# Optimization experiments

Hardware: AMD Instinct MI355X
Metric: run time of the kernel (lower is better)

The kernel has to match this reference:

```python
import jax, jax.numpy as jnp
import numpy as np

# SamplesLoss(loss='sinkhorn', p=1, blur=0.05): entropic regularization eps = blur**p = 0.05,
# debiased Sinkhorn divergence S(a,b) = OT(a,b) - 0.5*OT(a,a) - 0.5*OT(b,b).
EPS = 0.05
N_ITER = 50
N_POINTS = 32


def _cost(X, Y):
    # p=1 cost: Euclidean distance. X:[B,N,D] Y:[B,M,D] -> [B,N,M]
    d2 = jnp.sum((X[:, :, None, :] - Y[:, None, :, :]) ** 2, axis=-1)
    return jnp.sqrt(d2 + 1e-12)


def _ot(X, Y):
    # log-domain Sinkhorn with uniform weights; returns dual cost <mu,f>+<nu,g> per batch.
    B, N, _ = X.shape
    M = Y.shape[1]
    C = _cost(X, Y)  # [B,N,M]
    log_mu = jnp.full((B, N), -np.log(N), C.dtype)
    log_nu = jnp.full((B, M), -np.log(M), C.dtype)

    def body(carry, _):
        f, g = carry
        f = -EPS * jax.nn.logsumexp((g[:, None, :] - C) / EPS + log_nu[:, None, :], axis=2)
        g = -EPS * jax.nn.logsumexp((f[:, :, None] - C) / EPS + log_mu[:, :, None], axis=1)
        return (f, g), None

    init = (jnp.zeros((B, N), C.dtype), jnp.zeros((B, M), C.dtype))
    (f, g), _ = jax.lax.scan(body, init, None, length=N_ITER)
    return jnp.mean(f, axis=-1) + jnp.mean(g, axis=-1)  # uniform weights => mean


def _sinkhorn_div(X, Y):
    return _ot(X, Y) - 0.5 * _ot(X, X) - 0.5 * _ot(Y, Y)


def _encode(x, W, edge_index):
    # simple 1-layer GCN-style encoder: linear + mean neighbor aggregation + self, ReLU
    h = x @ W  # [n_nodes, emb_dim]
    src, dst = edge_index[0], edge_index[1]
    n = x.shape[0]
    agg = jax.ops.segment_sum(h[src], dst, num_segments=n)
    deg = jax.ops.segment_sum(jnp.ones(src.shape, h.dtype), dst, num_segments=n)
    return jax.nn.relu(h + agg / jnp.maximum(deg, 1.0)[:, None])


def setup_inputs() -> dict:
    key = jax.random.key(0)
    k1, k2, k3, k4, k5 = jax.random.split(key, 5)
    n_nodes, d_feat, emb_dim = 50000, 128, 256
    n_edges, n_pairs = 800000, 8192
    x = jax.random.normal(k1, (n_nodes, d_feat), jnp.float32)
    W = jax.random.normal(k2, (d_feat, emb_dim), jnp.float32) / np.sqrt(d_feat)
    edge_index = jax.random.randint(k3, (2, n_edges), 0, n_nodes, jnp.int64)
    pairs = jax.random.randint(k4, (2, n_pairs), 0, n_nodes, jnp.int64)
    graph_dist = jax.random.uniform(k5, (n_pairs,), jnp.float32, 1.0, 5.0)
    return {"x": x, "W": W, "edge_index": edge_index, "pairs": pairs,
            "graph_dist": graph_dist}


def reference(x, W, edge_index, pairs, graph_dist):
    z = _encode(x, W, edge_index)                       # [n_nodes, emb_dim]
    B = pairs.shape[1]
    Xa = z[pairs[0]].reshape(B, N_POINTS, -1)           # [B, n_points, space_dim]
    Xb = z[pairs[1]].reshape(B, N_POINTS, -1)
    distance = _sinkhorn_div(Xa, Xb)                    # = -score_pairs
    distortion = jnp.abs(distance - graph_dist) / graph_dist
    return jnp.mean(distortion)
```

## Files before the change

kernel.cpp:

```cpp
#include <hip/hip_runtime.h>

#define N_NODES 50000
#define N_EDGES 800000
#define N_PAIRS 8192
#define N_SLOTS (2 * N_PAIRS)
#define CAP     64

#define INV_EPS   20.0f
#define LOG2E_F   1.4426950408889634f
#define LN2_F     0.6931471805599453f
#define LN32_F    3.4657359027997265f
#define EPS_F     0.05f

typedef float f2 __attribute__((ext_vector_type(2)));

__global__ void k_mark(const int* __restrict__ pairs, int* __restrict__ flags) {
    int t = blockIdx.x * 256 + threadIdx.x;
    if (t < N_SLOTS) flags[pairs[t]] = 1;
}

__global__ __launch_bounds__(256) void k_scatter(
        const int* __restrict__ eidx, const int* __restrict__ flags,
        int* __restrict__ cnt, int* __restrict__ bucket) {
    int t = blockIdx.x * 256 + threadIdx.x;
    int dst = eidx[N_EDGES + t];
    if (!flags[dst]) return;
    int pos = atomicAdd(&cnt[dst], 1);
    if (pos < CAP) bucket[dst * CAP + pos] = eidx[t];
}

__global__ __launch_bounds__(256) void k_gemm(
        const int* __restrict__ pairs, const float* __restrict__ x,
        const int* __restrict__ cnt, const int* __restrict__ bucket,
        const float* __restrict__ W, float* __restrict__ Z) {
    __shared__ __align__(16) float Us[16 * 128];
    int sbase = blockIdx.x * 16;
    int t = threadIdx.x;
    int wave = t >> 6, lane = t & 63;

    #pragma unroll
    for (int rr = 0; rr < 4; ++rr) {
        int r = wave * 4 + rr;
        int node = pairs[sbase + r];
        int n = cnt[node];
        int m = (n < CAP) ? n : CAP;
        const int* bk = bucket + node * CAP;
        float ax = 0.0f, ay = 0.0f;
        int k = 0;
        for (; k + 4 <= m; k += 4) {
            int s0 = bk[k], s1 = bk[k + 1], s2 = bk[k + 2], s3 = bk[k + 3];
            float2 v0 = *(const float2*)(x + (size_t)s0 * 128 + lane * 2);
            float2 v1 = *(const float2*)(x + (size_t)s1 * 128 + lane * 2);
            float2 v2 = *(const float2*)(x + (size_t)s2 * 128 + lane * 2);
            float2 v3 = *(const float2*)(x + (size_t)s3 * 128 + lane * 2);
            ax += (v0.x + v1.x) + (v2.x + v3.x);
            ay += (v0.y + v1.y) + (v2.y + v3.y);
        }
        for (; k < m; ++k) {
            int s0 = bk[k];
            float2 v0 = *(const float2*)(x + (size_t)s0 * 128 + lane * 2);
            ax += v0.x;
            ay += v0.y;
        }
        float rdeg = 1.0f / fmaxf((float)n, 1.0f);
        float2 xv = *(const float2*)(x + (size_t)node * 128 + lane * 2);
        float2 o;
        o.x = fmaf(ax, rdeg, xv.x);
        o.y = fmaf(ay, rdeg, xv.y);
        *(float2*)(Us + r * 128 + lane * 2) = o;
    }
    __syncthreads();

    int jq = t & 63;
    int rq = t >> 6;
    float acc[4][4] = {};
    const float4* Wv = (const float4*)W;

    for (int k4 = 0; k4 < 32; ++k4) {
        float4 wv[4];
        #pragma unroll
        for (int i = 0; i < 4; ++i) wv[i] = Wv[(size_t)(k4 * 4 + i) * 64 + jq];
        #pragma unroll
        for (int r = 0; r < 4; ++r) {
            float4 uv = *(const float4*)(Us + (rq * 4 + r) * 128 + k4 * 4);
            float uk0 = uv.x, uk1 = uv.y, uk2 = uv.z, uk3 = uv.w;
            acc[r][0] = fmaf(uk0, wv[0].x, acc[r][0]);
            acc[r][1] = fmaf(uk0, wv[0].y, acc[r][1]);
            acc[r][2] = fmaf(uk0, wv[0].z, acc[r][2]);
            acc[r][3] = fmaf(uk0, wv[0].w, acc[r][3]);
            acc[r][0] = fmaf(uk1, wv[1].x, acc[r][0]);
            acc[r][1] = fmaf(uk1, wv[1].y, acc[r][1]);
            acc[r][2] = fmaf(uk1, wv[1].z, acc[r][2]);
            acc[r][3] = fmaf(uk1, wv[1].w, acc[r][3]);
            acc[r][0] = fmaf(uk2, wv[2].x, acc[r][0]);
            acc[r][1] = fmaf(uk2, wv[2].y, acc[r][1]);
            acc[r][2] = fmaf(uk2, wv[2].z, acc[r][2]);
            acc[r][3] = fmaf(uk2, wv[2].w, acc[r][3]);
            acc[r][0] = fmaf(uk3, wv[3].x, acc[r][0]);
            acc[r][1] = fmaf(uk3, wv[3].y, acc[r][1]);
            acc[r][2] = fmaf(uk3, wv[3].z, acc[r][2]);
            acc[r][3] = fmaf(uk3, wv[3].w, acc[r][3]);
        }
    }

    #pragma unroll
    for (int r = 0; r < 4; ++r) {
        float4 o;
        o.x = fmaxf(acc[r][0], 0.0f);
        o.y = fmaxf(acc[r][1], 0.0f);
        o.z = fmaxf(acc[r][2], 0.0f);
        o.w = fmaxf(acc[r][3], 0.0f);
        *(float4*)(Z + (size_t)(sbase + rq * 4 + r) * 256 + jq * 4) = o;
    }
}

__global__ __launch_bounds__(256) void k_sinkhorn(
        const float* __restrict__ Z, float* __restrict__ dist) {
    __shared__ __align__(16) float sX[4][256];
    __shared__ __align__(16) float sY[4][256];
    __shared__ __align__(16) float sf[4][32];
    __shared__ __align__(16) float sg[4][32];
    __shared__ __align__(16) float su[4][32];
    __shared__ __align__(16) float sv[4][32];

    int w = threadIdx.x >> 6;
    int lane = threadIdx.x & 63;
    int task = blockIdx.x * 4 + w;
    int b = task / 3;
    int kind = task - 3 * b;
    int sx = (kind == 2) ? (N_PAIRS + b) : b;
    int sy = (kind == 1) ? b : (N_PAIRS + b);

    *(float4*)(&sX[w][lane * 4]) = ((const float4*)(Z + (size_t)sx * 256))[lane];
    *(float4*)(&sY[w][lane * 4]) = ((const float4*)(Z + (size_t)sy * 256))[lane];
    sg[w][lane & 31] = 0.0f;

    const float CSCALE = -INV_EPS * LOG2E_F;
    const float CBIAS  = -LN32_F * LOG2E_F;

    int i_r = lane & 31, jh = lane >> 5;
    int j_c = lane & 31, ih = lane >> 5;

    f2 CrowV[8], CcolV[8];
    {
        const f2* xp = (const f2*)(&sX[w][i_r * 8]);
        f2 x0 = xp[0], x1 = xp[1], x2 = xp[2], x3 = xp[3];
        #pragma unroll
        for (int t = 0; t < 16; ++t) {
            int j = jh * 16 + t;
            const f2* yp = (const f2*)(&sY[w][j * 8]);
            f2 d, s2;
            d = x0 - yp[0]; s2 = d * d;
            d = x1 - yp[1]; s2 = __builtin_elementwise_fma(d, d, s2);
            d = x2 - yp[2]; s2 = __builtin_elementwise_fma(d, d, s2);
            d = x3 - yp[3]; s2 = __builtin_elementwise_fma(d, d, s2);
            float d2 = s2.x + s2.y + 1e-12f;
            CrowV[t >> 1][t & 1] = fmaf(__builtin_amdgcn_sqrtf(d2), CSCALE, CBIAS);
        }
        const f2* yp = (const f2*)(&sY[w][j_c * 8]);
        f2 y0 = yp[0], y1 = yp[1], y2 = yp[2], y3 = yp[3];
        #pragma unroll
        for (int t = 0; t < 16; ++t) {
            int i = ih * 16 + t;
            const f2* qp = (const f2*)(&sX[w][i * 8]);
            f2 d, s2;
            d = qp[0] - y0; s2 = d * d;
            d = qp[1] - y1; s2 = __builtin_elementwise_fma(d, d, s2);
            d = qp[2] - y2; s2 = __builtin_elementwise_fma(d, d, s2);
            d = qp[3] - y3; s2 = __builtin_elementwise_fma(d, d, s2);
            float d2 = s2.x + s2.y + 1e-12f;
            CcolV[t >> 1][t & 1] = fmaf(__builtin_amdgcn_sqrtf(d2), CSCALE, CBIAS);
        }
    }

    float ft = 0.0f, gt = 0.0f;

    #pragma unroll 1
    for (int it = 0; it < 2; ++it) {
        {
            const float4* gp = (const float4*)(&sg[w][jh * 16]);
            float4 G0 = gp[0], G1 = gp[1], G2 = gp[2], G3 = gp[3];
            f2 gv[8] = {f2{G0.x, G0.y}, f2{G0.z, G0.w}, f2{G1.x, G1.y}, f2{G1.z, G1.w},
                        f2{G2.x, G2.y}, f2{G2.z, G2.w}, f2{G3.x, G3.y}, f2{G3.z, G3.w}};
            f2 val[8], m2 = f2{-1e30f, -1e30f};
            #pragma unroll
            for (int t2 = 0; t2 < 8; ++t2) {
                val[t2] = gv[t2] + CrowV[t2];
                m2 = __builtin_elementwise_max(m2, val[t2]);
            }
            float m = fmaxf(m2.x, m2.y);
            m = fmaxf(m, __shfl_xor(m, 32));
            f2 mm = f2{m, m};
            float s0 = 0.0f, s1 = 0.0f;
            #pragma unroll
            for (int t2 = 0; t2 < 8; ++t2) {
                f2 e = val[t2] - mm;
                s0 += __builtin_amdgcn_exp2f(e.x);
                s1 += __builtin_amdgcn_exp2f(e.y);
            }
            float s = s0 + s1;
            s += __shfl_xor(s, 32);
            ft = -(m + __builtin_amdgcn_logf(s));
        }
        sf[w][lane & 31] = ft;
        {
            const float4* fp = (const float4*)(&sf[w][ih * 16]);
            float4 F0 = fp[0], F1 = fp[1], F2 = fp[2], F3 = fp[3];
            f2 fv[8] = {f2{F0.x, F0.y}, f2{F0.z, F0.w}, f2{F1.x, F1.y}, f2{F1.z, F1.w},
                        f2{F2.x, F2.y}, f2{F2.z, F2.w}, f2{F3.x, F3.y}, f2{F3.z, F3.w}};
            f2 val[8], m2 = f2{-1e30f, -1e30f};
            #pragma unroll
            for (int t2 = 0; t2 < 8; ++t2) {
                val[t2] = fv[t2] + CcolV[t2];
                m2 = __builtin_elementwise_max(m2, val[t2]);
            }
            float m = fmaxf(m2.x, m2.y);
            m = fmaxf(m, __shfl_xor(m, 32));
            f2 mm = f2{m, m};
            float s0 = 0.0f, s1 = 0.0f;
            #pragma unroll
            for (int t2 = 0; t2 < 8; ++t2) {
                f2 e = val[t2] - mm;
                s0 += __builtin_amdgcn_exp2f(e.x);
                s1 += __builtin_amdgcn_exp2f(e.y);
            }
            float s = s0 + s1;
            s += __shfl_xor(s, 32);
            gt = -(m + __builtin_amdgcn_logf(s));
        }
        sg[w][lane & 31] = gt;
    }

    f2 KR2[8], KC2[8];
    float ureg = 1.0f, vreg = 1.0f;

    auto absorb = [&]() {
        const float4* gp = (const float4*)(&sg[w][jh * 16]);
        float4 G0 = gp[0], G1 = gp[1], G2 = gp[2], G3 = gp[3];
        f2 gv[8] = {f2{G0.x, G0.y}, f2{G0.z, G0.w}, f2{G1.x, G1.y}, f2{G1.z, G1.w},
                    f2{G2.x, G2.y}, f2{G2.z, G2.w}, f2{G3.x, G3.y}, f2{G3.z, G3.w}};
        f2 ftv = f2{ft, ft};
        #pragma unroll
        for (int t2 = 0; t2 < 8; ++t2) {
            f2 a = (gv[t2] + CrowV[t2]) + ftv;
            KR2[t2].x = __builtin_amdgcn_exp2f(a.x);
            KR2[t2].y = __builtin_amdgcn_exp2f(a.y);
        }
        const float4* fp = (const float4*)(&sf[w][ih * 16]);
        float4 F0 = fp[0], F1 = fp[1], F2 = fp[2], F3 = fp[3];
        f2 fv[8] = {f2{F0.x, F0.y}, f2{F0.z, F0.w}, f2{F1.x, F1.y}, f2{F1.z, F1.w},
                    f2{F2.x, F2.y}, f2{F2.z, F2.w}, f2{F3.x, F3.y}, f2{F3.z, F3.w}};
        f2 gtv = f2{gt, gt};
        #pragma unroll
        for (int t2 = 0; t2 < 8; ++t2) {
            f2 a = (fv[t2] + CcolV[t2]) + gtv;
            KC2[t2].x = __builtin_amdgcn_exp2f(a.x);
            KC2[t2].y = __builtin_amdgcn_exp2f(a.y);
        }
        sv[w][lane & 31] = 1.0f;
        ureg = 1.0f;
        vreg = 1.0f;
    };

    const int blens[5] = {6, 6, 12, 12, 12};
    absorb();
    #pragma unroll 1
    for (int blk = 0; blk < 5; ++blk) {
        int L = blens[blk];
        #pragma unroll 2
        for (int s6 = 0; s6 < L; ++s6) {
            {
                const float4* vp = (const float4*)(&sv[w][jh * 16]);
                float4 A0 = vp[0], A1 = vp[1], A2 = vp[2], A3 = vp[3];
                f2 acc0 = KR2[0] * f2{A0.x, A0.y};
                f2 acc1 = KR2[1] * f2{A0.z, A0.w};
                acc0 = __builtin_elementwise_fma(KR2[2], f2{A1.x, A1.y}, acc0);
                acc1 = __builtin_elementwise_fma(KR2[3], f2{A1.z, A1.w}, acc1);
                acc0 = __builtin_elementwise_fma(KR2[4], f2{A2.x, A2.y}, acc0);
                acc1 = __builtin_elementwise_fma(KR2[5], f2{A2.z, A2.w}, acc1);
                acc0 = __builtin_elementwise_fma(KR2[6], f2{A3.x, A3.y}, acc0);
                acc1 = __builtin_elementwise_fma(KR2[7], f2{A3.z, A3.w}, acc1);
                f2 a = acc0 + acc1;
                float S = a.x + a.y;
                S += __shfl_xor(S, 32);
                ureg = __builtin_amdgcn_rcpf(S);
            }
            su[w][lane & 31] = ureg;
            {
                const float4* up = (const float4*)(&su[w][ih * 16]);
                float4 A0 = up[0], A1 = up[1], A2 = up[2], A3 = up[3];
                f2 acc0 = KC2[0] * f2{A0.x, A0.y};
                f2 acc1 = KC2[1] * f2{A0.z, A0.w};
                acc0 = __builtin_elementwise_fma(KC2[2], f2{A1.x, A1.y}, acc0);
                acc1 = __builtin_elementwise_fma(KC2[3], f2{A1.z, A1.w}, acc1);
                acc0 = __builtin_elementwise_fma(KC2[4], f2{A2.x, A2.y}, acc0);
                acc1 = __builtin_elementwise_fma(KC2[5], f2{A2.z, A2.w}, acc1);
                acc0 = __builtin_elementwise_fma(KC2[6], f2{A3.x, A3.y}, acc0);
                acc1 = __builtin_elementwise_fma(KC2[7], f2{A3.z, A3.w}, acc1);
                f2 a = acc0 + acc1;
                float T = a.x + a.y;
                T += __shfl_xor(T, 32);
                vreg = __builtin_amdgcn_rcpf(T);
            }
            sv[w][lane & 31] = vreg;
        }
        if (blk < 4) {
            ft += __builtin_amdgcn_logf(ureg);
            gt += __builtin_amdgcn_logf(vreg);
            sf[w][lane & 31] = ft;
            sg[w][lane & 31] = gt;
            absorb();
        }
    }
    ft += __builtin_amdgcn_logf(ureg);
    gt += __builtin_amdgcn_logf(vreg);

    float v = ft + gt;
    #pragma unroll
    for (int off = 32; off > 0; off >>= 1) v += __shfl_xor(v, off);
    if (lane == 0) {
        float cost = v * (EPS_F * LN2_F / 64.0f);
        float wgt = (kind == 0) ? 1.0f : -0.5f;
        unsafeAtomicAdd(&dist[b], wgt * cost);
    }
}

__global__ void k_finalize(const float* __restrict__ dist,
                           const float* __restrict__ gd, float* __restrict__ out) {
    __shared__ float red[256];
    float s = 0.0f;
    for (int i = threadIdx.x; i < N_PAIRS; i += 256) {
        float g = gd[i];
        s += fabsf(dist[i] - g) / g;
    }
    red[threadIdx.x] = s;
    __syncthreads();
    for (int o = 128; o > 0; o >>= 1) {
        if (threadIdx.x < o) red[threadIdx.x] += red[threadIdx.x + o];
        __syncthreads();
    }
    if (threadIdx.x == 0) out[0] = red[0] * (1.0f / N_PAIRS);
}

extern "C" void kernel_launch(void* const* d_in, const int* in_sizes, int n_in,
                              void* d_out, int out_size, void* d_ws, size_t ws_size,
                              hipStream_t stream) {
    const float* x    = (const float*)d_in[0];
    const float* W    = (const float*)d_in[1];
    const int*   eidx = (const int*)d_in[2];
    const int*   pair = (const int*)d_in[3];
    const float* gd   = (const float*)d_in[4];

    char* ws = (char*)d_ws;
    size_t off = 0;
    int*   cnt    = (int*)  (ws + off); off += (size_t)N_NODES * 4;
    int*   flags  = (int*)  (ws + off); off += (size_t)N_NODES * 4;
    float* dist   = (float*)(ws + off); off += (size_t)N_PAIRS * 4;
    size_t zero_bytes = off;
    int*   bucket = (int*)  (ws + off); off += (size_t)N_NODES * CAP * 4;
    float* Z      = (float*)(ws + off); off += (size_t)N_SLOTS * 256 * 4;

    hipMemsetAsync(d_ws, 0, zero_bytes, stream);
    k_mark    <<<(N_SLOTS + 255) / 256, 256, 0, stream>>>(pair, flags);
    k_scatter <<<N_EDGES / 256, 256, 0, stream>>>(eidx, flags, cnt, bucket);
    k_gemm    <<<N_SLOTS / 16, 256, 0, stream>>>(pair, x, cnt, bucket, W, Z);
    k_sinkhorn<<<(3 * N_PAIRS) / 4, 256, 0, stream>>>(Z, dist);
    k_finalize<<<1, 256, 0, stream>>>(dist, gd, (float*)d_out);
}
```

Baseline: 292.7 us.

## Specialize symmetric self-OT Sinkhorn tasks to half-wave symmetric iterations

The Sinkhorn kernel now splits blocks into cross-pair tasks (X vs Y) and self tasks (X vs X, Y vs Y). Self tasks use the symmetry of the cost matrix, so a single scaling vector updated by one matvec per half-step covers the problem, and each 64-lane wave handles both self-OT problems of a pair, one per 32-lane half. The total number of waves drops from three per pair to two, with less work per self problem. The risk is numerical: the symmetric single-vector iteration and its final averaging of the last two iterates must match the alternating f/g updates of the reference.

```diff
diff --git a/kernel.cpp b/kernel.cpp
--- a/kernel.cpp
+++ b/kernel.cpp
@@ -116,212 +116,314 @@
 
 __global__ __launch_bounds__(256) void k_sinkhorn(
         const float* __restrict__ Z, float* __restrict__ dist) {
-    __shared__ __align__(16) float sX[4][256];
-    __shared__ __align__(16) float sY[4][256];
-    __shared__ __align__(16) float sf[4][32];
-    __shared__ __align__(16) float sg[4][32];
-    __shared__ __align__(16) float su[4][32];
-    __shared__ __align__(16) float sv[4][32];
+    __shared__ __align__(16) float smem[4][640];
 
     int w = threadIdx.x >> 6;
     int lane = threadIdx.x & 63;
-    int task = blockIdx.x * 4 + w;
-    int b = task / 3;
-    int kind = task - 3 * b;
-    int sx = (kind == 2) ? (N_PAIRS + b) : b;
-    int sy = (kind == 1) ? b : (N_PAIRS + b);
-
-    *(float4*)(&sX[w][lane * 4]) = ((const float4*)(Z + (size_t)sx * 256))[lane];
-    *(float4*)(&sY[w][lane * 4]) = ((const float4*)(Z + (size_t)sy * 256))[lane];
-    sg[w][lane & 31] = 0.0f;
-
     const float CSCALE = -INV_EPS * LOG2E_F;
     const float CBIAS  = -LN32_F * LOG2E_F;
 
-    int i_r = lane & 31, jh = lane >> 5;
-    int j_c = lane & 31, ih = lane >> 5;
-
-    f2 CrowV[8], CcolV[8];
-    {
-        const f2* xp = (const f2*)(&sX[w][i_r * 8]);
-        f2 x0 = xp[0], x1 = xp[1], x2 = xp[2], x3 = xp[3];
-        #pragma unroll
-        for (int t = 0; t < 16; ++t) {
-            int j = jh * 16 + t;
-            const f2* yp = (const f2*)(&sY[w][j * 8]);
-            f2 d, s2;
-            d = x0 - yp[0]; s2 = d * d;
-            d = x1 - yp[1]; s2 = __builtin_elementwise_fma(d, d, s2);
-            d = x2 - yp[2]; s2 = __builtin_elementwise_fma(d, d, s2);
-            d = x3 - yp[3]; s2 = __builtin_elementwise_fma(d, d, s2);
-            float d2 = s2.x + s2.y + 1e-12f;
-            CrowV[t >> 1][t & 1] = fmaf(__builtin_amdgcn_sqrtf(d2), CSCALE, CBIAS);
-        }
-        const f2* yp = (const f2*)(&sY[w][j_c * 8]);
-        f2 y0 = yp[0], y1 = yp[1], y2 = yp[2], y3 = yp[3];
-        #pragma unroll
-        for (int t = 0; t < 16; ++t) {
-            int i = ih * 16 + t;
-            const f2* qp = (const f2*)(&sX[w][i * 8]);
-            f2 d, s2;
-            d = qp[0] - y0; s2 = d * d;
-            d = qp[1] - y1; s2 = __builtin_elementwise_fma(d, d, s2);
-            d = qp[2] - y2; s2 = __builtin_elementwise_fma(d, d, s2);
-            d = qp[3] - y3; s2 = __builtin_elementwise_fma(d, d, s2);
-            float d2 = s2.x + s2.y + 1e-12f;
-            CcolV[t >> 1][t & 1] = fmaf(__builtin_amdgcn_sqrtf(d2), CSCALE, CBIAS);
-        }
-    }
-
-    float ft = 0.0f, gt = 0.0f;
-
-    #pragma unroll 1
-    for (int it = 0; it < 2; ++it) {
+    if (blockIdx.x < 2048) {
+        float* sX = &smem[w][0];
+        float* sY = &smem[w][256];
+        float* sf = &smem[w][512];
+        float* sg = &smem[w][544];
+        float* su = &smem[w][576];
+        float* sv = &smem[w][608];
+
+        int b = blockIdx.x * 4 + w;
+        int sx = b, sy = N_PAIRS + b;
+
+        *(float4*)(&sX[lane * 4]) = ((const float4*)(Z + (size_t)sx * 256))[lane];
+        *(float4*)(&sY[lane * 4]) = ((const float4*)(Z + (size_t)sy * 256))[lane];
+        sg[lane & 31] = 0.0f;
+
+        int i_r = lane & 31, jh = lane >> 5;
+        int j_c = lane & 31, ih = lane >> 5;
+
+        f2 CrowV[8], CcolV[8];
         {
-            const float4* gp = (const float4*)(&sg[w][jh * 16]);
+            const f2* xp = (const f2*)(&sX[i_r * 8]);
+            f2 x0 = xp[0], x1 = xp[1], x2 = xp[2], x3 = xp[3];
+            #pragma unroll
+            for (int t = 0; t < 16; ++t) {
+                int j = jh * 16 + t;
+                const f2* yp = (const f2*)(&sY[j * 8]);
+                f2 d, s2;
+                d = x0 - yp[0]; s2 = d * d;
+                d = x1 - yp[1]; s2 = __builtin_elementwise_fma(d, d, s2);
+                d = x2 - yp[2]; s2 = __builtin_elementwise_fma(d, d, s2);
+                d = x3 - yp[3]; s2 = __builtin_elementwise_fma(d, d, s2);
+                float d2 = s2.x + s2.y + 1e-12f;
+                CrowV[t >> 1][t & 1] = fmaf(__builtin_amdgcn_sqrtf(d2), CSCALE, CBIAS);
+            }
+            const f2* yp = (const f2*)(&sY[j_c * 8]);
+            f2 y0 = yp[0], y1 = yp[1], y2 = yp[2], y3 = yp[3];
+            #pragma unroll
+            for (int t = 0; t < 16; ++t) {
+                int i = ih * 16 + t;
+                const f2* qp = (const f2*)(&sX[i * 8]);
+                f2 d, s2;
+                d = qp[0] - y0; s2 = d * d;
+                d = qp[1] - y1; s2 = __builtin_elementwise_fma(d, d, s2);
+                d = qp[2] - y2; s2 = __builtin_elementwise_fma(d, d, s2);
+                d = qp[3] - y3; s2 = __builtin_elementwise_fma(d, d, s2);
+                float d2 = s2.x + s2.y + 1e-12f;
+                CcolV[t >> 1][t & 1] = fmaf(__builtin_amdgcn_sqrtf(d2), CSCALE, CBIAS);
+            }
+        }
+
+        float ft = 0.0f, gt = 0.0f;
+
+        #pragma unroll 1
+        for (int it = 0; it < 2; ++it) {
+            {
+                const float4* gp = (const float4*)(&sg[jh * 16]);
+                float4 G0 = gp[0], G1 = gp[1], G2 = gp[2], G3 = gp[3];
+                f2 gv[8] = {f2{G0.x, G0.y}, f2{G0.z, G0.w}, f2{G1.x, G1.y}, f2{G1.z, G1.w},
+                            f2{G2.x, G2.y}, f2{G2.z, G2.w}, f2{G3.x, G3.y}, f2{G3.z, G3.w}};
+                f2 val[8], m2 = f2{-1e30f, -1e30f};
+                #pragma unroll
+                for (int t2 = 0; t2 < 8; ++t2) {
+                    val[t2] = gv[t2] + CrowV[t2];
+                    m2 = __builtin_elementwise_max(m2, val[t2]);
+                }
+                float m = fmaxf(m2.x, m2.y);
+                m = fmaxf(m, __shfl_xor(m, 32));
+                f2 mm = f2{m, m};
+                float s0 = 0.0f, s1 = 0.0f;
+                #pragma unroll
+                for (int t2 = 0; t2 < 8; ++t2) {
+                    f2 e = val[t2] - mm;
+                    s0 += __builtin_amdgcn_exp2f(e.x);
+                    s1 += __builtin_amdgcn_exp2f(e.y);
+                }
+                float s = s0 + s1;
+                s += __shfl_xor(s, 32);
+                ft = -(m + __builtin_amdgcn_logf(s));
+            }
+            sf[lane & 31] = ft;
+            {
+                const float4* fp = (const float4*)(&sf[ih * 16]);
+                float4 F0 = fp[0], F1 = fp[1], F2 = fp[2], F3 = fp[3];
+                f2 fv[8] = {f2{F0.x, F0.y}, f2{F0.z, F0.w}, f2{F1.x, F1.y}, f2{F1.z, F1.w},
+                            f2{F2.x, F2.y}, f2{F2.z, F2.w}, f2{F3.x, F3.y}, f2{F3.z, F3.w}};
+                f2 val[8], m2 = f2{-1e30f, -1e30f};
+                #pragma unroll
+                for (int t2 = 0; t2 < 8; ++t2) {
+                    val[t2] = fv[t2] + CcolV[t2];
+                    m2 = __builtin_elementwise_max(m2, val[t2]);
+                }
+                float m = fmaxf(m2.x, m2.y);
+                m = fmaxf(m, __shfl_xor(m, 32));
+                f2 mm = f2{m, m};
+                float s0 = 0.0f, s1 = 0.0f;
+                #pragma unroll
+                for (int t2 = 0; t2 < 8; ++t2) {
+                    f2 e = val[t2] - mm;
+                    s0 += __builtin_amdgcn_exp2f(e.x);
+                    s1 += __builtin_amdgcn_exp2f(e.y);
+                }
+                float s = s0 + s1;
+                s += __shfl_xor(s, 32);
+                gt = -(m + __builtin_amdgcn_logf(s));
+            }
+            sg[lane & 31] = gt;
+        }
+
+        f2 KR2[8], KC2[8];
+        float ureg = 1.0f, vreg = 1.0f;
+
+        auto absorb = [&]() {
+            const float4* gp = (const float4*)(&sg[jh * 16]);
             float4 G0 = gp[0], G1 = gp[1], G2 = gp[2], G3 = gp[3];
             f2 gv[8] = {f2{G0.x, G0.y}, f2{G0.z, G0.w}, f2{G1.x, G1.y}, f2{G1.z, G1.w},
                         f2{G2.x, G2.y}, f2{G2.z, G2.w}, f2{G3.x, G3.y}, f2{G3.z, G3.w}};
-            f2 val[8], m2 = f2{-1e30f, -1e30f};
+            f2 ftv = f2{ft, ft};
             #pragma unroll
             for (int t2 = 0; t2 < 8; ++t2) {
-                val[t2] = gv[t2] + CrowV[t2];
-                m2 = __builtin_elementwise_max(m2, val[t2]);
-            }
-            float m = fmaxf(m2.x, m2.y);
-            m = fmaxf(m, __shfl_xor(m, 32));
-            f2 mm = f2{m, m};
-            float s0 = 0.0f, s1 = 0.0f;
-            #pragma unroll
-            for (int t2 = 0; t2 < 8; ++t2) {
-                f2 e = val[t2] - mm;
-                s0 += __builtin_amdgcn_exp2f(e.x);
-                s1 += __builtin_amdgcn_exp2f(e.y);
-            }
-            float s = s0 + s1;
-            s += __shfl_xor(s, 32);
-            ft = -(m + __builtin_amdgcn_logf(s));
-        }
-        sf[w][lane & 31] = ft;
-        {
-            const float4* fp = (const float4*)(&sf[w][ih * 16]);
+                f2 a = (gv[t2] + CrowV[t2]) + ftv;
+                KR2[t2].x = __builtin_amdgcn_exp2f(a.x);
+                KR2[t2].y = __builtin_amdgcn_exp2f(a.y);
+            }
+            const float4* fp = (const float4*)(&sf[ih * 16]);
             float4 F0 = fp[0], F1 = fp[1], F2 = fp[2], F3 = fp[3];
             f2 fv[8] = {f2{F0.x, F0.y}, f2{F0.z, F0.w}, f2{F1.x, F1.y}, f2{F1.z, F1.w},
                         f2{F2.x, F2.y}, f2{F2.z, F2.w}, f2{F3.x, F3.y}, f2{F3.z, F3.w}};
-            f2 val[8], m2 = f2{-1e30f, -1e30f};
+            f2 gtv = f2{gt, gt};
             #pragma unroll
             for (int t2 = 0; t2 < 8; ++t2) {
-                val[t2] = fv[t2] + CcolV[t2];
-                m2 = __builtin_elementwise_max(m2, val[t2]);
-            }
-            float m = fmaxf(m2.x, m2.y);
-            m = fmaxf(m, __shfl_xor(m, 32));
-            f2 mm = f2{m, m};
-            float s0 = 0.0f, s1 = 0.0f;
+                f2 a = (fv[t2] + CcolV[t2]) + gtv;
+                KC2[t2].x = __builtin_amdgcn_exp2f(a.x);
+                KC2[t2].y = __builtin_amdgcn_exp2f(a.y);
+            }
+            sv[lane & 31] = 1.0f;
+            ureg = 1.0f;
+            vreg = 1.0f;
+        };
+
+        const int blens[5] = {6, 6, 12, 12, 12};
+        absorb();
+        #pragma unroll 1
+        for (int blk = 0; blk < 5; ++blk) {
+            int L = blens[blk];
+            #pragma unroll 2
+            for (int s6 = 0; s6 < L; ++s6) {
+                {
+                    const float4* vp = (const float4*)(&sv[jh * 16]);
+                    float4 A0 = vp[0], A1 = vp[1], A2 = vp[2], A3 = vp[3];
+                    f2 acc0 = KR2[0] * f2{A0.x, A0.y};
+                    f2 acc1 = KR2[1] * f2{A0.z, A0.w};
+                    acc0 = __builtin_elementwise_fma(KR2[2], f2{A1.x, A1.y}, acc0);
+                    acc1 = __builtin_elementwise_fma(KR2[3], f2{A1.z, A1.w}, acc1);
+                    acc0 = __builtin_elementwise_fma(KR2[4], f2{A2.x, A2.y}, acc0);
+                    acc1 = __builtin_elementwise_fma(KR2[5], f2{A2.z, A2.w}, acc1);
+                    acc0 = __builtin_elementwise_fma(KR2[6], f2{A3.x, A3.y}, acc0);
+                    acc1 = __builtin_elementwise_fma(KR2[7], f2{A3.z, A3.w}, acc1);
+                    f2 a = acc0 + acc1;
+                    float S = a.x + a.y;
+                    S += __shfl_xor(S, 32);
+                    ureg = __builtin_amdgcn_rcpf(S);
+                }
+                su[lane & 31] = ureg;
+                {
+                    const float4* up = (const float4*)(&su[ih * 16]);
+                    float4 A0 = up[0], A1 = up[1], A2 = up[2], A3 = up[3];
+                    f2 acc0 = KC2[0] * f2{A0.x, A0.y};
+                    f2 acc1 = KC2[1] * f2{A0.z, A0.w};
+                    acc0 = __builtin_elementwise_fma(KC2[2], f2{A1.x, A1.y}, acc0);
+                    acc1 = __builtin_elementwise_fma(KC2[3], f2{A1.z, A1.w}, acc1);
+                    acc0 = __builtin_elementwise_fma(KC2[4], f2{A2.x, A2.y}, acc0);
+                    acc1 = __builtin_elementwise_fma(KC2[5], f2{A2.z, A2.w}, acc1);
+                    acc0 = __builtin_elementwise_fma(KC2[6], f2{A3.x, A3.y}, acc0);
+                    acc1 = __builtin_elementwise_fma(KC2[7], f2{A3.z, A3.w}, acc1);
+                    f2 a = acc0 + acc1;
+                    float T = a.x + a.y;
+                    T += __shfl_xor(T, 32);
+                    vreg = __builtin_amdgcn_rcpf(T);
+                }
+                sv[lane & 31] = vreg;
+            }
+            if (blk < 4) {
+                ft += __builtin_amdgcn_logf(ureg);
+                gt += __builtin_amdgcn_logf(vreg);
+                sf[lane & 31] = ft;
+                sg[lane & 31] = gt;
+                absorb();
+            }
+        }
+        ft += __builtin_amdgcn_logf(ureg);
+        gt += __builtin_amdgcn_logf(vreg);
+
+        float v = ft + gt;
+        #pragma unroll
+        for (int off = 32; off > 0; off >>= 1) v += __shfl_xor(v, off);
+        if (lane == 0) {
+            float cost = v * (EPS_F * LN2_F / 64.0f);
+            unsafeAtomicAdd(&dist[b], cost);
+        }
+    } else {
+        int h = lane >> 5, i = lane & 31;
+        int P = (blockIdx.x - 2048) * 4 + w;
+        int src = h ? (N_PAIRS + P) : P;
+
+        float* sP  = &smem[w][h * 256];
+        float* swv = &smem[w][512];
+        float* spv = &smem[w][576];
+
+        {
+            const float4* zp = (const float4*)(Z + (size_t)src * 256);
+            *(float4*)(&sP[i * 8])     = zp[i * 2];
+            *(float4*)(&sP[i * 8 + 4]) = zp[i * 2 + 1];
+        }
+
+        f2 CV[16];
+        {
+            const f2* xp = (const f2*)(&sP[i * 8]);
+            f2 x0 = xp[0], x1 = xp[1], x2 = xp[2], x3 = xp[3];
             #pragma unroll
-            for (int t2 = 0; t2 < 8; ++t2) {
-                f2 e = val[t2] - mm;
-                s0 += __builtin_amdgcn_exp2f(e.x);
-                s1 += __builtin_amdgcn_exp2f(e.y);
-            }
-            float s = s0 + s1;
-            s += __shfl_xor(s, 32);
-            gt = -(m + __builtin_amdgcn_logf(s));
-        }
-        sg[w][lane & 31] = gt;
-    }
-
-    f2 KR2[8], KC2[8];
-    float ureg = 1.0f, vreg = 1.0f;
-
-    auto absorb = [&]() {
-        const float4* gp = (const float4*)(&sg[w][jh * 16]);
-        float4 G0 = gp[0], G1 = gp[1], G2 = gp[2], G3 = gp[3];
-        f2 gv[8] = {f2{G0.x, G0.y}, f2{G0.z, G0.w}, f2{G1.x, G1.y}, f2{G1.z, G1.w},
-                    f2{G2.x, G2.y}, f2{G2.z, G2.w}, f2{G3.x, G3.y}, f2{G3.z, G3.w}};
-        f2 ftv = f2{ft, ft};
+            for (int j = 0; j < 32; ++j) {
+                const f2* yp = (const f2*)(&sP[j * 8]);
+                f2 d, s2;
+                d = x0 - yp[0]; s2 = d * d;
+                d = x1 - yp[1]; s2 = __builtin_elementwise_fma(d, d, s2);
+                d = x2 - yp[2]; s2 = __builtin_elementwise_fma(d, d, s2);
+                d = x3 - yp[3]; s2 = __builtin_elementwise_fma(d, d, s2);
+                float d2 = s2.x + s2.y + 1e-12f;
+                CV[j >> 1][j & 1] = fmaf(__builtin_amdgcn_sqrtf(d2), CSCALE, CBIAS);
+            }
+        }
+
+        float pp = 0.0f, E = 1.0f, wcur = 1.0f, wprev = 1.0f;
+        f2 KV[16];
         #pragma unroll
-        for (int t2 = 0; t2 < 8; ++t2) {
-            f2 a = (gv[t2] + CrowV[t2]) + ftv;
-            KR2[t2].x = __builtin_amdgcn_exp2f(a.x);
-            KR2[t2].y = __builtin_amdgcn_exp2f(a.y);
-        }
-        const float4* fp = (const float4*)(&sf[w][ih * 16]);
-        float4 F0 = fp[0], F1 = fp[1], F2 = fp[2], F3 = fp[3];
-        f2 fv[8] = {f2{F0.x, F0.y}, f2{F0.z, F0.w}, f2{F1.x, F1.y}, f2{F1.z, F1.w},
-                    f2{F2.x, F2.y}, f2{F2.z, F2.w}, f2{F3.x, F3.y}, f2{F3.z, F3.w}};
-        f2 gtv = f2{gt, gt};
-        #pragma unroll
-        for (int t2 = 0; t2 < 8; ++t2) {
-            f2 a = (fv[t2] + CcolV[t2]) + gtv;
-            KC2[t2].x = __builtin_amdgcn_exp2f(a.x);
-            KC2[t2].y = __builtin_amdgcn_exp2f(a.y);
-        }
-        sv[w][lane & 31] = 1.0f;
-        ureg = 1.0f;
-        vreg = 1.0f;
-    };
-
-    const int blens[5] = {6, 6, 12, 12, 12};
-    absorb();
-    #pragma unroll 1
-    for (int blk = 0; blk < 5; ++blk) {
-        int L = blens[blk];
-        #pragma unroll 2
-        for (int s6 = 0; s6 < L; ++s6) {
-            {
-                const float4* vp = (const float4*)(&sv[w][jh * 16]);
-                float4 A0 = vp[0], A1 = vp[1], A2 = vp[2], A3 = vp[3];
-                f2 acc0 = KR2[0] * f2{A0.x, A0.y};
-                f2 acc1 = KR2[1] * f2{A0.z, A0.w};
-                acc0 = __builtin_elementwise_fma(KR2[2], f2{A1.x, A1.y}, acc0);
-                acc1 = __builtin_elementwise_fma(KR2[3], f2{A1.z, A1.w}, acc1);
-                acc0 = __builtin_elementwise_fma(KR2[4], f2{A2.x, A2.y}, acc0);
-                acc1 = __builtin_elementwise_fma(KR2[5], f2{A2.z, A2.w}, acc1);
-                acc0 = __builtin_elementwise_fma(KR2[6], f2{A3.x, A3.y}, acc0);
-                acc1 = __builtin_elementwise_fma(KR2[7], f2{A3.z, A3.w}, acc1);
+        for (int t = 0; t < 16; ++t) {
+            KV[t].x = __builtin_amdgcn_exp2f(CV[t].x);
+            KV[t].y = __builtin_amdgcn_exp2f(CV[t].y);
+        }
+        swv[lane] = 1.0f;
+
+        const int blens[9] = {4, 12, 12, 12, 12, 12, 12, 12, 12};
+        #pragma unroll 1
+        for (int blk = 0; blk < 9; ++blk) {
+            int L = blens[blk];
+            #pragma unroll 2
+            for (int s = 0; s < L; ++s) {
+                const float4* wp = (const float4*)(&swv[h * 32]);
+                float4 A0 = wp[0], A1 = wp[1], A2 = wp[2], A3 = wp[3];
+                float4 A4 = wp[4], A5 = wp[5], A6 = wp[6], A7 = wp[7];
+                f2 acc0 = KV[0] * f2{A0.x, A0.y};
+                f2 acc1 = KV[1] * f2{A0.z, A0.w};
+                acc0 = __builtin_elementwise_fma(KV[2],  f2{A1.x, A1.y}, acc0);
+                acc1 = __builtin_elementwise_fma(KV[3],  f2{A1.z, A1.w}, acc1);
+                acc0 = __builtin_elementwise_fma(KV[4],  f2{A2.x, A2.y}, acc0);
+                acc1 = __builtin_elementwise_fma(KV[5],  f2{A2.z, A2.w}, acc1);
+                acc0 = __builtin_elementwise_fma(KV[6],  f2{A3.x, A3.y}, acc0);
+                acc1 = __builtin_elementwise_fma(KV[7],  f2{A3.z, A3.w}, acc1);
+                acc0 = __builtin_elementwise_fma(KV[8],  f2{A4.x, A4.y}, acc0);
+                acc1 = __builtin_elementwise_fma(KV[9],  f2{A4.z, A4.w}, acc1);
+                acc0 = __builtin_elementwise_fma(KV[10], f2{A5.x, A5.y}, acc0);
+                acc1 = __builtin_elementwise_fma(KV[11], f2{A5.z, A5.w}, acc1);
+                acc0 = __builtin_elementwise_fma(KV[12], f2{A6.x, A6.y}, acc0);
+                acc1 = __builtin_elementwise_fma(KV[13], f2{A6.z, A6.w}, acc1);
+                acc0 = __builtin_elementwise_fma(KV[14], f2{A7.x, A7.y}, acc0);
+                acc1 = __builtin_elementwise_fma(KV[15], f2{A7.z, A7.w}, acc1);
                 f2 a = acc0 + acc1;
                 float S = a.x + a.y;
-                S += __shfl_xor(S, 32);
-                ureg = __builtin_amdgcn_rcpf(S);
-            }
-            su[w][lane & 31] = ureg;
-            {
-                const float4* up = (const float4*)(&su[w][ih * 16]);
-                float4 A0 = up[0], A1 = up[1], A2 = up[2], A3 = up[3];
-                f2 acc0 = KC2[0] * f2{A0.x, A0.y};
-                f2 acc1 = KC2[1] * f2{A0.z, A0.w};
-                acc0 = __builtin_elementwise_fma(KC2[2], f2{A1.x, A1.y}, acc0);
-                acc1 = __builtin_elementwise_fma(KC2[3], f2{A1.z, A1.w}, acc1);
-                acc0 = __builtin_elementwise_fma(KC2[4], f2{A2.x, A2.y}, acc0);
-                acc1 = __builtin_elementwise_fma(KC2[5], f2{A2.z, A2.w}, acc1);
-                acc0 = __builtin_elementwise_fma(KC2[6], f2{A3.x, A3.y}, acc0);
-                acc1 = __builtin_elementwise_fma(KC2[7], f2{A3.z, A3.w}, acc1);
-                f2 a = acc0 + acc1;
-                float T = a.x + a.y;
-                T += __shfl_xor(T, 32);
-                vreg = __builtin_amdgcn_rcpf(T);
-            }
-            sv[w][lane & 31] = vreg;
-        }
-        if (blk < 4) {
-            ft += __builtin_amdgcn_logf(ureg);
-            gt += __builtin_amdgcn_logf(vreg);
-            sf[w][lane & 31] = ft;
-            sg[w][lane & 31] = gt;
-            absorb();
-        }
-    }
-    ft += __builtin_amdgcn_logf(ureg);
-    gt += __builtin_amdgcn_logf(vreg);
-
-    float v = ft + gt;
-    #pragma unroll
-    for (int off = 32; off > 0; off >>= 1) v += __shfl_xor(v, off);
-    if (lane == 0) {
-        float cost = v * (EPS_F * LN2_F / 64.0f);
-        float wgt = (kind == 0) ? 1.0f : -0.5f;
-        unsafeAtomicAdd(&dist[b], wgt * cost);
+                wprev = wcur;
+                wcur = __builtin_amdgcn_rcpf(S) * E;
+                swv[h * 32 + i] = wcur;
+            }
+            if (blk < 8) {
+                pp += __builtin_amdgcn_logf(wcur);
+                spv[lane] = pp;
+                const float4* pv = (const float4*)(&spv[h * 32]);
+                float4 P0 = pv[0], P1 = pv[1], P2 = pv[2], P3 = pv[3];
+                float4 P4 = pv[4], P5 = pv[5], P6 = pv[6], P7 = pv[7];
+                f2 pj[16] = {f2{P0.x,P0.y}, f2{P0.z,P0.w}, f2{P1.x,P1.y}, f2{P1.z,P1.w},
+                             f2{P2.x,P2.y}, f2{P2.z,P2.w}, f2{P3.x,P3.y}, f2{P3.z,P3.w},
+                             f2{P4.x,P4.y}, f2{P4.z,P4.w}, f2{P5.x,P5.y}, f2{P5.z,P5.w},
+                             f2{P6.x,P6.y}, f2{P6.z,P6.w}, f2{P7.x,P7.y}, f2{P7.z,P7.w}};
+                #pragma unroll
+                for (int t = 0; t < 16; ++t) {
+                    f2 a = pj[t] + CV[t];
+                    KV[t].x = __builtin_amdgcn_exp2f(a.x);
+                    KV[t].y = __builtin_amdgcn_exp2f(a.y);
+                }
+                E = __builtin_amdgcn_exp2f(-pp);
+                wcur = 1.0f;
+                swv[lane] = 1.0f;
+            }
+        }
+
+        float zsum = 2.0f * pp + __builtin_amdgcn_logf(wprev)
+                   + __builtin_amdgcn_logf(wcur);
+        #pragma unroll
+        for (int off = 16; off > 0; off >>= 1) zsum += __shfl_xor(zsum, off);
+        if (i == 0) {
+            float cost = zsum * (EPS_F * LN2_F / 32.0f);
+            unsafeAtomicAdd(&dist[P], -0.5f * cost);
+        }
     }
 }
 
@@ -364,6 +466,6 @@
     k_mark    <<<(N_SLOTS + 255) / 256, 256, 0, stream>>>(pair, flags);
     k_scatter <<<N_EDGES / 256, 256, 0, stream>>>(eidx, flags, cnt, bucket);
     k_gemm    <<<N_SLOTS / 16, 256, 0, stream>>>(pair, x, cnt, bucket, W, Z);
-    k_sinkhorn<<<(3 * N_PAIRS) / 4, 256, 0, stream>>>(Z, dist);
+    k_sinkhorn<<<4096, 256, 0, stream>>>(Z, dist);
     k_finalize<<<1, 256, 0, stream>>>(dist, gd, (float*)d_out);
 }
```

New measurement: 261.6 us. 1.12x faster.
